# Optimization experiments

Hardware: AMD Instinct MI355X
Metric: run time of the kernel (lower is better)

Reference implementation:

```python
import jax, jax.numpy as jnp
import numpy as np

D_MODEL = 1024
N_HEADS = 16
D_K = D_MODEL // N_HEADS


def setup_inputs() -> dict:
    key = jax.random.key(0)
    ks = jax.random.split(key, 9)
    B, S = 2, 2048
    scale = 1.0 / np.sqrt(D_MODEL)
    inp = {
        "X": jax.random.normal(ks[0], (B, S, D_MODEL), dtype=jnp.float32),
        "Wq": jax.random.normal(ks[1], (D_MODEL, D_MODEL), dtype=jnp.float32) * scale,
        "bq": jnp.zeros((D_MODEL,), dtype=jnp.float32),
        "Wk": jax.random.normal(ks[2], (D_MODEL, D_MODEL), dtype=jnp.float32) * scale,
        "bk": jnp.zeros((D_MODEL,), dtype=jnp.float32),
        "Wv": jax.random.normal(ks[3], (D_MODEL, D_MODEL), dtype=jnp.float32) * scale,
        "bv": jnp.zeros((D_MODEL,), dtype=jnp.float32),
        "Wo": jax.random.normal(ks[4], (D_MODEL, D_MODEL), dtype=jnp.float32) * scale,
        "bo": jnp.zeros((D_MODEL,), dtype=jnp.float32),
    }
    return inp


def reference(X, Wq, bq, Wk, bk, Wv, bv, Wo, bo):
    B, S, _ = X.shape
    # QKV projections (torch Linear: x @ W.T + b; here W stored as [in, out])
    Q = X @ Wq + bq
    K = X @ Wk + bk
    V = X @ Wv + bv
    # [B, S, H, Dk] -> [B, H, S, Dk]
    def split_heads(t):
        return t.reshape(B, S, N_HEADS, D_K).transpose(0, 2, 1, 3)
    Q, K, V = split_heads(Q), split_heads(K), split_heads(V)
    scores = jnp.einsum('bhqd,bhkd->bhqk', Q, K) / jnp.sqrt(jnp.float32(D_K))
    attn = jax.nn.softmax(scores, axis=-1)
    out = jnp.einsum('bhqk,bhkd->bhqd', attn, V)  # [B, H, S, Dk]
    out = out.transpose(0, 2, 1, 3).reshape(B, S, D_MODEL)
    return out @ Wo + bo
```

## Files before the change

### kernel.cpp

```cpp
#include <hip/hip_runtime.h>
#include <hip/hip_bf16.h>


typedef __attribute__((ext_vector_type(8))) short short8;
typedef __attribute__((ext_vector_type(4))) float f32x4;
typedef unsigned short u16;
typedef unsigned int u32;

static __device__ __forceinline__ u16 f2bf(float f) {
    union { float f; u32 u; } c; c.f = f;
    u32 u = c.u;
    u32 r = u + 0x7fffu + ((u >> 16) & 1u);
    return (u16)(r >> 16);
}
static __device__ __forceinline__ float bf2f(u16 x) {
    union { u32 u; float f; } c; c.u = ((u32)x) << 16;
    return c.f;
}

#define GL1(p) ((const __attribute__((address_space(1))) void*)(p))
#define LD3(p) ((__attribute__((address_space(3))) void*)(p))
static __device__ __forceinline__ void gld16(const void* g, void* l) {
    __builtin_amdgcn_global_load_lds(GL1(g), LD3(l), 16, 0, 0);
}

#define Q_PRESCALE 0.18033688011112042f

__global__ __launch_bounds__(256) void prep(
    const float* __restrict__ X, u16* __restrict__ Xb,
    const float* __restrict__ W0, const float* __restrict__ W1,
    const float* __restrict__ W2, const float* __restrict__ W3,
    u16* __restrict__ T0, u16* __restrict__ T1,
    u16* __restrict__ T2, u16* __restrict__ T3)
{
    int id = blockIdx.x;
    int t = threadIdx.x;
    if (id >= 1024) {
        int i = (id - 1024) * 1024 + t * 4;
        float4 v = *reinterpret_cast<const float4*>(X + i);
        ushort4 o;
        o.x = f2bf(v.x); o.y = f2bf(v.y); o.z = f2bf(v.z); o.w = f2bf(v.w);
        *reinterpret_cast<ushort4*>(Xb + i) = o;
        return;
    }
    const float* W; u16* T;
    switch (id >> 8) {
        case 0: W = W0; T = T0; break;
        case 1: W = W1; T = T1; break;
        case 2: W = W2; T = T2; break;
        default: W = W3; T = T3; break;
    }
    int rem = id & 255;
    int n0 = (rem & 15) * 64, k0 = (rem >> 4) * 64;
    __shared__ float tile[64][65];
    int r = t / 16, c4 = (t % 16) * 4;
    #pragma unroll
    for (int p = 0; p < 4; p++) {
        int row = p * 16 + r;
        float4 v = *reinterpret_cast<const float4*>(W + (k0 + row) * 1024 + n0 + c4);
        tile[row][c4 + 0] = v.x; tile[row][c4 + 1] = v.y;
        tile[row][c4 + 2] = v.z; tile[row][c4 + 3] = v.w;
    }
    __syncthreads();
    #pragma unroll
    for (int p = 0; p < 4; p++) {
        int nrow = p * 16 + r;
        ushort4 o;
        o.x = f2bf(tile[c4 + 0][nrow]); o.y = f2bf(tile[c4 + 1][nrow]);
        o.z = f2bf(tile[c4 + 2][nrow]); o.w = f2bf(tile[c4 + 3][nrow]);
        *reinterpret_cast<ushort4*>(T + (n0 + nrow) * 1024 + k0 + c4) = o;
    }
}

__global__ __launch_bounds__(256) void gemm_qkv(
    const u16* __restrict__ Xb,
    const u16* __restrict__ Wtq, const u16* __restrict__ Wtk, const u16* __restrict__ Wtv,
    const float* __restrict__ bq, const float* __restrict__ bk, const float* __restrict__ bv,
    u16* __restrict__ Qn, u16* __restrict__ Kn, u16* __restrict__ Vtg)
{
    const u16* Wt; const float* bias;
    if (blockIdx.z == 0)      { Wt = Wtq; bias = bq; }
    else if (blockIdx.z == 1) { Wt = Wtk; bias = bk; }
    else                      { Wt = Wtv; bias = bv; }

    __shared__ __align__(16) u16 As[128 * 32];
    __shared__ __align__(16) u16 Bs[128 * 32];
    int t = threadIdx.x;
    int w = t >> 6, lane = t & 63, l15 = lane & 15, quad = lane >> 4;
    int wm = (w >> 1) * 64, wn = (w & 1) * 64;
    int row0 = blockIdx.y * 128, col0 = blockIdx.x * 128;

    int drow = lane >> 2;
    int gc8 = ((lane & 3) ^ (drow & 3) ^ ((drow >> 2) & 3)) * 8;
    int asw = ((quad ^ (l15 & 3) ^ ((l15 >> 2) & 3)) & 3) * 8;

    f32x4 acc[4][4];
    #pragma unroll
    for (int i = 0; i < 4; i++)
        #pragma unroll
        for (int j = 0; j < 4; j++)
            acc[i][j] = (f32x4){0.f, 0.f, 0.f, 0.f};

    for (int k0 = 0; k0 < 1024; k0 += 32) {
        __syncthreads();
        #pragma unroll
        for (int q = 0; q < 2; q++) {
            int rr = w * 32 + q * 16;
            gld16(&Xb[(row0 + rr + drow) * 1024 + k0 + gc8], &As[rr * 32]);
            gld16(&Wt[(col0 + rr + drow) * 1024 + k0 + gc8], &Bs[rr * 32]);
        }
        __syncthreads();
        short8 a[4], b[4];
        #pragma unroll
        for (int i = 0; i < 4; i++)
            a[i] = *reinterpret_cast<const short8*>(&As[(wm + i * 16 + l15) * 32 + asw]);
        #pragma unroll
        for (int j = 0; j < 4; j++)
            b[j] = *reinterpret_cast<const short8*>(&Bs[(wn + j * 16 + l15) * 32 + asw]);
        #pragma unroll
        for (int i = 0; i < 4; i++)
            #pragma unroll
            for (int j = 0; j < 4; j++)
                acc[i][j] = __builtin_amdgcn_mfma_f32_16x16x32_bf16(a[i], b[j], acc[i][j], 0, 0, 0);
    }

    if (blockIdx.z == 2) {
        #pragma unroll
        for (int i = 0; i < 4; i++) {
            int gr = row0 + wm + i * 16 + quad * 4;
            int b_ = gr >> 11, s = gr & 2047;
            #pragma unroll
            for (int j = 0; j < 4; j++) {
                int col = col0 + wn + j * 16 + l15;
                int h = col >> 6, d = col & 63;
                float bb = bias[col];
                ushort4 pk;
                pk.x = f2bf(acc[i][j][0] + bb);
                pk.y = f2bf(acc[i][j][1] + bb);
                pk.z = f2bf(acc[i][j][2] + bb);
                pk.w = f2bf(acc[i][j][3] + bb);
                *reinterpret_cast<ushort4*>(&Vtg[((b_ * 16 + h) * 64 + d) * 2048 + s]) = pk;
            }
        }
    } else {
        u16* dst = (blockIdx.z == 0) ? Qn : Kn;
        float osc = (blockIdx.z == 0) ? Q_PRESCALE : 1.0f;
        #pragma unroll
        for (int i = 0; i < 4; i++) {
            int rowb = row0 + wm + i * 16 + quad * 4;
            #pragma unroll
            for (int j = 0; j < 4; j++) {
                int col = col0 + wn + j * 16 + l15;
                float bb = bias[col];
                #pragma unroll
                for (int r = 0; r < 4; r++)
                    dst[(rowb + r) * 1024 + col] = f2bf((acc[i][j][r] + bb) * osc);
            }
        }
    }
}

__global__ __launch_bounds__(256) void attn(
    const u16* __restrict__ Qn, const u16* __restrict__ Kn,
    const u16* __restrict__ Vtg, u16* __restrict__ Opart, float* __restrict__ Lsum)
{
    int qt = blockIdx.x, bh = blockIdx.y, sp = blockIdx.z;
    int b_ = bh >> 4, h = bh & 15;
    const u16* Vp = Vtg + bh * (64 * 2048);
    u16* Op = Opart + sp * (4096 * 1024);
    float* Lp = Lsum + sp * (32 * 2048) + bh * 2048;

    __shared__ __align__(16) u16 Ks[64 * 64];
    __shared__ __align__(16) u16 Vt[64 * 64];
    __shared__ __align__(16) u16 Ps[128 * 64];

    int t = threadIdx.x, w = t >> 6, lane = t & 63, l15 = lane & 15, quad = lane >> 4;

    short8 qf[2][2];
    #pragma unroll
    for (int f = 0; f < 2; f++)
        #pragma unroll
        for (int ds = 0; ds < 2; ds++)
            qf[f][ds] = *reinterpret_cast<const short8*>(
                &Qn[(b_ * 2048 + qt * 128 + w * 32 + f * 16 + l15) * 1024 +
                    h * 64 + ds * 32 + quad * 8]);

    int di = lane >> 3;
    int dc8 = ((lane & 7) ^ di) * 8;

    int rl = l15 & 7, rh = l15 >> 3;
    int koff[4][2];
    #pragma unroll
    for (int j = 0; j < 4; j++)
        #pragma unroll
        for (int ds = 0; ds < 2; ds++)
            koff[j][ds] = (j * 2 + rh) * 512 + rl * 64 + (((ds * 4 + quad) ^ rl) & 7) * 8;

    int pwt[2][4];
    #pragma unroll
    for (int f = 0; f < 2; f++)
        #pragma unroll
        for (int j = 0; j < 4; j++)
            pwt[f][j] = (w * 32 + f * 16 + l15) * 64 +
                        (((2 * j + (quad >> 1)) ^ rl) * 8) + (quad & 1) * 4;
    int prt[2][2];
    #pragma unroll
    for (int f = 0; f < 2; f++)
        #pragma unroll
        for (int ks = 0; ks < 2; ks++)
            prt[f][ks] = (w * 32 + f * 16 + l15) * 64 + (((4 * ks + quad) ^ rl) * 8);

    f32x4 acc[2][4];
    float lsum[2] = {0.f, 0.f};
    #pragma unroll
    for (int f = 0; f < 2; f++)
        #pragma unroll
        for (int j = 0; j < 4; j++) acc[f][j] = (f32x4){0.f, 0.f, 0.f, 0.f};

    for (int kt = 0; kt < 16; kt++) {
        int kbase = sp * 1024 + kt * 64;
        __syncthreads();
        #pragma unroll
        for (int sg = 0; sg < 2; sg++) {
            int seg = w * 2 + sg;
            gld16(&Kn[(b_ * 2048 + kbase + seg * 8 + di) * 1024 + h * 64 + dc8],
                  &Ks[seg * 512]);
            gld16(&Vp[(seg * 8 + di) * 2048 + kbase + dc8], &Vt[seg * 512]);
        }
        __syncthreads();

        f32x4 sc[2][4];
        #pragma unroll
        for (int j = 0; j < 4; j++) {
            f32x4 s0 = (f32x4){0.f, 0.f, 0.f, 0.f};
            f32x4 s1 = (f32x4){0.f, 0.f, 0.f, 0.f};
            #pragma unroll
            for (int ds = 0; ds < 2; ds++) {
                short8 kf = *reinterpret_cast<const short8*>(&Ks[koff[j][ds]]);
                s0 = __builtin_amdgcn_mfma_f32_16x16x32_bf16(kf, qf[0][ds], s0, 0, 0, 0);
                s1 = __builtin_amdgcn_mfma_f32_16x16x32_bf16(kf, qf[1][ds], s1, 0, 0, 0);
            }
            sc[0][j] = s0; sc[1][j] = s1;
        }

        #pragma unroll
        for (int f = 0; f < 2; f++)
            #pragma unroll
            for (int j = 0; j < 4; j++) {
                float p0 = __builtin_amdgcn_exp2f(sc[f][j][0]);
                float p1 = __builtin_amdgcn_exp2f(sc[f][j][1]);
                float p2 = __builtin_amdgcn_exp2f(sc[f][j][2]);
                float p3 = __builtin_amdgcn_exp2f(sc[f][j][3]);
                lsum[f] += (p0 + p1) + (p2 + p3);
                union { float fv; u32 uv; } c0, c1, c2, c3;
                c0.fv = p0; c1.fv = p1; c2.fv = p2; c3.fv = p3;
                uint2 pk;
                pk.x = (c0.uv >> 16) | (c1.uv & 0xffff0000u);
                pk.y = (c2.uv >> 16) | (c3.uv & 0xffff0000u);
                *reinterpret_cast<uint2*>(&Ps[pwt[f][j]]) = pk;
            }

        #pragma unroll
        for (int ks = 0; ks < 2; ks++) {
            short8 pf0 = *reinterpret_cast<const short8*>(&Ps[prt[0][ks]]);
            short8 pf1 = *reinterpret_cast<const short8*>(&Ps[prt[1][ks]]);
            #pragma unroll
            for (int j = 0; j < 4; j++) {
                short8 vf = *reinterpret_cast<const short8*>(&Vt[koff[j][ks]]);
                acc[0][j] = __builtin_amdgcn_mfma_f32_16x16x32_bf16(pf0, vf, acc[0][j], 0, 0, 0);
                acc[1][j] = __builtin_amdgcn_mfma_f32_16x16x32_bf16(pf1, vf, acc[1][j], 0, 0, 0);
            }
        }
    }

    #pragma unroll
    for (int f = 0; f < 2; f++) {
        float s = lsum[f];
        s += __shfl_xor(s, 16);
        s += __shfl_xor(s, 32);
        lsum[f] = s;
    }
    if (quad == 0) {
        #pragma unroll
        for (int f = 0; f < 2; f++)
            Lp[qt * 128 + w * 32 + f * 16 + l15] = lsum[f];
    }

    #pragma unroll
    for (int f = 0; f < 2; f++)
        #pragma unroll
        for (int j = 0; j < 4; j++)
            #pragma unroll
            for (int r = 0; r < 4; r++) {
                int srow = qt * 128 + w * 32 + f * 16 + quad * 4 + r;
                Op[(b_ * 2048 + srow) * 1024 + h * 64 + j * 16 + l15] = f2bf(acc[f][j][r]);
            }
}

__global__ __launch_bounds__(256) void combine(
    const u16* __restrict__ O0, const u16* __restrict__ O1,
    const float* __restrict__ L0, const float* __restrict__ L1,
    u16* __restrict__ Ob)
{
    int idx8 = (blockIdx.x * 256 + threadIdx.x) * 8;
    int row = idx8 >> 10, col = idx8 & 1023;
    int b_ = row >> 11, s = row & 2047, h = col >> 6;
    int li = (b_ * 16 + h) * 2048 + s;
    float inv = 1.0f / (L0[li] + L1[li]);
    union { uint4 v; u16 s[8]; } ua, ub, uo;
    ua.v = *reinterpret_cast<const uint4*>(&O0[idx8]);
    ub.v = *reinterpret_cast<const uint4*>(&O1[idx8]);
    #pragma unroll
    for (int i = 0; i < 8; i++)
        uo.s[i] = f2bf((bf2f(ua.s[i]) + bf2f(ub.s[i])) * inv);
    *reinterpret_cast<uint4*>(&Ob[idx8]) = uo.v;
}

__global__ __launch_bounds__(256) void gemm_out(
    const u16* __restrict__ Ob, const u16* __restrict__ Wto,
    const float* __restrict__ bo, float* __restrict__ out)
{
    __shared__ __align__(16) u16 As[128 * 32];
    __shared__ __align__(16) u16 Bs[128 * 32];
    int t = threadIdx.x;
    int w = t >> 6, lane = t & 63, l15 = lane & 15, quad = lane >> 4;
    int wm = (w >> 1) * 64, wn = (w & 1) * 64;
    int row0 = blockIdx.y * 128, col0 = blockIdx.x * 128;

    int drow = lane >> 2;
    int gc8 = ((lane & 3) ^ (drow & 3) ^ ((drow >> 2) & 3)) * 8;
    int asw = ((quad ^ (l15 & 3) ^ ((l15 >> 2) & 3)) & 3) * 8;

    f32x4 acc[4][4];
    #pragma unroll
    for (int i = 0; i < 4; i++)
        #pragma unroll
        for (int j = 0; j < 4; j++)
            acc[i][j] = (f32x4){0.f, 0.f, 0.f, 0.f};

    for (int k0 = 0; k0 < 1024; k0 += 32) {
        __syncthreads();
        #pragma unroll
        for (int q = 0; q < 2; q++) {
            int rr = w * 32 + q * 16;
            gld16(&Ob[(row0 + rr + drow) * 1024 + k0 + gc8], &As[rr * 32]);
            gld16(&Wto[(col0 + rr + drow) * 1024 + k0 + gc8], &Bs[rr * 32]);
        }
        __syncthreads();
        short8 a[4], b[4];
        #pragma unroll
        for (int i = 0; i < 4; i++)
            a[i] = *reinterpret_cast<const short8*>(&As[(wm + i * 16 + l15) * 32 + asw]);
        #pragma unroll
        for (int j = 0; j < 4; j++)
            b[j] = *reinterpret_cast<const short8*>(&Bs[(wn + j * 16 + l15) * 32 + asw]);
        #pragma unroll
        for (int i = 0; i < 4; i++)
            #pragma unroll
            for (int j = 0; j < 4; j++)
                acc[i][j] = __builtin_amdgcn_mfma_f32_16x16x32_bf16(a[i], b[j], acc[i][j], 0, 0, 0);
    }
    #pragma unroll
    for (int i = 0; i < 4; i++) {
        int rowb = row0 + wm + i * 16 + quad * 4;
        #pragma unroll
        for (int j = 0; j < 4; j++) {
            int col = col0 + wn + j * 16 + l15;
            float bb = bo[col];
            #pragma unroll
            for (int r = 0; r < 4; r++)
                out[(rowb + r) * 1024 + col] = acc[i][j][r] + bb;
        }
    }
}

extern "C" void kernel_launch(void* const* d_in, const int* in_sizes, int n_in,
                              void* d_out, int out_size, void* d_ws, size_t ws_size,
                              hipStream_t stream) {
    const float* X  = (const float*)d_in[0];
    const float* Wq = (const float*)d_in[1];
    const float* bq = (const float*)d_in[2];
    const float* Wk = (const float*)d_in[3];
    const float* bk = (const float*)d_in[4];
    const float* Wv = (const float*)d_in[5];
    const float* bv = (const float*)d_in[6];
    const float* Wo = (const float*)d_in[7];
    const float* bo = (const float*)d_in[8];
    float* out = (float*)d_out;

    char* ws = (char*)d_ws;
    u16* Xb   = (u16*)(ws);
    u16* Wtq  = (u16*)(ws + (8u  << 20));
    u16* Wtk  = (u16*)(ws + (10u << 20));
    u16* Wtv  = (u16*)(ws + (12u << 20));
    u16* Wto  = (u16*)(ws + (14u << 20));
    u16* Qn   = (u16*)(ws + (16u << 20));
    u16* Kn   = (u16*)(ws + (24u << 20));
    u16* Vtg  = (u16*)(ws + (32u << 20));
    u16* Op   = (u16*)(ws + (40u << 20));
    float* Ls = (float*)(ws + (56u << 20));
    u16* Ob   = (u16*)(ws + (57u << 20));

    prep     <<<5120, 256, 0, stream>>>(X, Xb, Wq, Wk, Wv, Wo, Wtq, Wtk, Wtv, Wto);
    gemm_qkv <<<dim3(8, 32, 3), 256, 0, stream>>>(Xb, Wtq, Wtk, Wtv, bq, bk, bv, Qn, Kn, Vtg);
    attn     <<<dim3(16, 32, 2), 256, 0, stream>>>(Qn, Kn, Vtg, Op, Ls);
    combine  <<<2048, 256, 0, stream>>>(Op, Op + (4096 * 1024), Ls, Ls + (32 * 2048), Ob);
    gemm_out <<<dim3(8, 32), 256, 0, stream>>>(Ob, Wto, bo, out);
}
```

Measured before the change: 234.2 us.

## Double-buffer LDS tiles, fuse QKV GEMM, and store Q/K head-major

Converts the QKV GEMM, output GEMM and attention K/V loops to a double-buffered LDS scheme with one barrier per iteration, prefetching the next tile while computing the current one. Concatenates Wq/Wk/Wv into one transposed matrix with the Q scale folded into weights and bias, launching a flat 1D grid. Q and K are written in [B,H,S,Dk] layout so attention loads contiguous per-head rows. Uses more LDS per block and relies on the barrier's implicit wait for async global-to-LDS loads.

Result: faster. 212.1 us (-9.4%).

```diff
diff --git a/kernel.cpp b/kernel.cpp
--- a/kernel.cpp
+++ b/kernel.cpp
@@ -28,13 +28,22 @@
 
 __global__ __launch_bounds__(256) void prep(
     const float* __restrict__ X, u16* __restrict__ Xb,
-    const float* __restrict__ W0, const float* __restrict__ W1,
-    const float* __restrict__ W2, const float* __restrict__ W3,
-    u16* __restrict__ T0, u16* __restrict__ T1,
-    u16* __restrict__ T2, u16* __restrict__ T3)
+    const float* __restrict__ Wq, const float* __restrict__ Wk,
+    const float* __restrict__ Wv, const float* __restrict__ Wo,
+    const float* __restrict__ bq, const float* __restrict__ bk,
+    const float* __restrict__ bv,
+    u16* __restrict__ Wqkv, u16* __restrict__ Wto, float* __restrict__ Bp)
 {
     int id = blockIdx.x;
     int t = threadIdx.x;
+    if (id == 5120) {
+        for (int i = t; i < 3072; i += 256) {
+            int wsel = i >> 10, c = i & 1023;
+            float v = (wsel == 0) ? bq[c] * Q_PRESCALE : (wsel == 1 ? bk[c] : bv[c]);
+            Bp[i] = v;
+        }
+        return;
+    }
     if (id >= 1024) {
         int i = (id - 1024) * 1024 + t * 4;
         float4 v = *reinterpret_cast<const float4*>(X + i);
@@ -43,12 +52,13 @@
         *reinterpret_cast<ushort4*>(Xb + i) = o;
         return;
     }
-    const float* W; u16* T;
-    switch (id >> 8) {
-        case 0: W = W0; T = T0; break;
-        case 1: W = W1; T = T1; break;
-        case 2: W = W2; T = T2; break;
-        default: W = W3; T = T3; break;
+    int which = id >> 8;
+    const float* W; u16* T; float sc;
+    switch (which) {
+        case 0: W = Wq; T = Wqkv;                sc = Q_PRESCALE; break;
+        case 1: W = Wk; T = Wqkv + 1024 * 1024;  sc = 1.0f; break;
+        case 2: W = Wv; T = Wqkv + 2048 * 1024;  sc = 1.0f; break;
+        default: W = Wo; T = Wto;                sc = 1.0f; break;
     }
     int rem = id & 255;
     int n0 = (rem & 15) * 64, k0 = (rem >> 4) * 64;
@@ -58,8 +68,8 @@
     for (int p = 0; p < 4; p++) {
         int row = p * 16 + r;
         float4 v = *reinterpret_cast<const float4*>(W + (k0 + row) * 1024 + n0 + c4);
-        tile[row][c4 + 0] = v.x; tile[row][c4 + 1] = v.y;
-        tile[row][c4 + 2] = v.z; tile[row][c4 + 3] = v.w;
+        tile[row][c4 + 0] = v.x * sc; tile[row][c4 + 1] = v.y * sc;
+        tile[row][c4 + 2] = v.z * sc; tile[row][c4 + 3] = v.w * sc;
     }
     __syncthreads();
     #pragma unroll
@@ -72,28 +82,26 @@
     }
 }
 
-__global__ __launch_bounds__(256) void gemm_qkv(
-    const u16* __restrict__ Xb,
-    const u16* __restrict__ Wtq, const u16* __restrict__ Wtk, const u16* __restrict__ Wtv,
-    const float* __restrict__ bq, const float* __restrict__ bk, const float* __restrict__ bv,
-    u16* __restrict__ Qn, u16* __restrict__ Kn, u16* __restrict__ Vtg)
+__global__ __launch_bounds__(256, 3) void gemm_qkv(
+    const u16* __restrict__ Xb, const u16* __restrict__ Wqkv,
+    const float* __restrict__ Bp,
+    u16* __restrict__ Qb, u16* __restrict__ Kb, u16* __restrict__ Vtg)
 {
-    const u16* Wt; const float* bias;
-    if (blockIdx.z == 0)      { Wt = Wtq; bias = bq; }
-    else if (blockIdx.z == 1) { Wt = Wtk; bias = bk; }
-    else                      { Wt = Wtv; bias = bv; }
-
-    __shared__ __align__(16) u16 As[128 * 32];
-    __shared__ __align__(16) u16 Bs[128 * 32];
+    __shared__ __align__(16) u16 As[2][128 * 32];
+    __shared__ __align__(16) u16 Bs[2][128 * 32];
     int t = threadIdx.x;
     int w = t >> 6, lane = t & 63, l15 = lane & 15, quad = lane >> 4;
     int wm = (w >> 1) * 64, wn = (w & 1) * 64;
-    int row0 = blockIdx.y * 128, col0 = blockIdx.x * 128;
+    int bid = blockIdx.x;
+    int row0 = (bid / 24) * 128, col0 = (bid % 24) * 128;
 
     int drow = lane >> 2;
     int gc8 = ((lane & 3) ^ (drow & 3) ^ ((drow >> 2) & 3)) * 8;
     int asw = ((quad ^ (l15 & 3) ^ ((l15 >> 2) & 3)) & 3) * 8;
 
+    const u16* Ag = Xb + (row0 + drow) * 1024 + gc8;
+    const u16* Bg = Wqkv + (col0 + drow) * 1024 + gc8;
+
     f32x4 acc[4][4];
     #pragma unroll
     for (int i = 0; i < 4; i++)
@@ -101,22 +109,31 @@
         for (int j = 0; j < 4; j++)
             acc[i][j] = (f32x4){0.f, 0.f, 0.f, 0.f};
 
-    for (int k0 = 0; k0 < 1024; k0 += 32) {
+    #pragma unroll
+    for (int q = 0; q < 2; q++) {
+        int rr = w * 32 + q * 16;
+        gld16(Ag + rr * 1024, &As[0][rr * 32]);
+        gld16(Bg + rr * 1024, &Bs[0][rr * 32]);
+    }
+    for (int kt = 0; kt < 32; kt++) {
         __syncthreads();
-        #pragma unroll
-        for (int q = 0; q < 2; q++) {
-            int rr = w * 32 + q * 16;
-            gld16(&Xb[(row0 + rr + drow) * 1024 + k0 + gc8], &As[rr * 32]);
-            gld16(&Wt[(col0 + rr + drow) * 1024 + k0 + gc8], &Bs[rr * 32]);
-        }
-        __syncthreads();
+        int cur = kt & 1;
+        if (kt < 31) {
+            int k0 = (kt + 1) * 32;
+            #pragma unroll
+            for (int q = 0; q < 2; q++) {
+                int rr = w * 32 + q * 16;
+                gld16(Ag + rr * 1024 + k0, &As[cur ^ 1][rr * 32]);
+                gld16(Bg + rr * 1024 + k0, &Bs[cur ^ 1][rr * 32]);
+            }
+        }
         short8 a[4], b[4];
         #pragma unroll
         for (int i = 0; i < 4; i++)
-            a[i] = *reinterpret_cast<const short8*>(&As[(wm + i * 16 + l15) * 32 + asw]);
-        #pragma unroll
-        for (int j = 0; j < 4; j++)
-            b[j] = *reinterpret_cast<const short8*>(&Bs[(wn + j * 16 + l15) * 32 + asw]);
+            a[i] = *reinterpret_cast<const short8*>(&As[cur][(wm + i * 16 + l15) * 32 + asw]);
+        #pragma unroll
+        for (int j = 0; j < 4; j++)
+            b[j] = *reinterpret_cast<const short8*>(&Bs[cur][(wn + j * 16 + l15) * 32 + asw]);
         #pragma unroll
         for (int i = 0; i < 4; i++)
             #pragma unroll
@@ -124,7 +141,8 @@
                 acc[i][j] = __builtin_amdgcn_mfma_f32_16x16x32_bf16(a[i], b[j], acc[i][j], 0, 0, 0);
     }
 
-    if (blockIdx.z == 2) {
+    int osel = col0 >> 10;
+    if (osel == 2) {
         #pragma unroll
         for (int i = 0; i < 4; i++) {
             int gr = row0 + wm + i * 16 + quad * 4;
@@ -132,8 +150,8 @@
             #pragma unroll
             for (int j = 0; j < 4; j++) {
                 int col = col0 + wn + j * 16 + l15;
-                int h = col >> 6, d = col & 63;
-                float bb = bias[col];
+                int c = col & 1023, h = c >> 6, d = c & 63;
+                float bb = Bp[col];
                 ushort4 pk;
                 pk.x = f2bf(acc[i][j][0] + bb);
                 pk.y = f2bf(acc[i][j][1] + bb);
@@ -143,35 +161,40 @@
             }
         }
     } else {
-        u16* dst = (blockIdx.z == 0) ? Qn : Kn;
-        float osc = (blockIdx.z == 0) ? Q_PRESCALE : 1.0f;
+        u16* dst = osel ? Kb : Qb;
         #pragma unroll
         for (int i = 0; i < 4; i++) {
             int rowb = row0 + wm + i * 16 + quad * 4;
             #pragma unroll
             for (int j = 0; j < 4; j++) {
                 int col = col0 + wn + j * 16 + l15;
-                float bb = bias[col];
+                int c = col & 1023, h = c >> 6, d = c & 63;
+                float bb = Bp[col];
                 #pragma unroll
-                for (int r = 0; r < 4; r++)
-                    dst[(rowb + r) * 1024 + col] = f2bf((acc[i][j][r] + bb) * osc);
+                for (int r = 0; r < 4; r++) {
+                    int gr = rowb + r;
+                    int b_ = gr >> 11, s = gr & 2047;
+                    dst[(((b_ << 4) + h) * 2048 + s) * 64 + d] = f2bf(acc[i][j][r] + bb);
+                }
             }
         }
     }
 }
 
 __global__ __launch_bounds__(256) void attn(
-    const u16* __restrict__ Qn, const u16* __restrict__ Kn,
+    const u16* __restrict__ Qb, const u16* __restrict__ Kb,
     const u16* __restrict__ Vtg, u16* __restrict__ Opart, float* __restrict__ Lsum)
 {
     int qt = blockIdx.x, bh = blockIdx.y, sp = blockIdx.z;
     int b_ = bh >> 4, h = bh & 15;
+    const u16* Qp = Qb + bh * (2048 * 64);
+    const u16* Kp = Kb + bh * (2048 * 64);
     const u16* Vp = Vtg + bh * (64 * 2048);
     u16* Op = Opart + sp * (4096 * 1024);
     float* Lp = Lsum + sp * (32 * 2048) + bh * 2048;
 
-    __shared__ __align__(16) u16 Ks[64 * 64];
-    __shared__ __align__(16) u16 Vt[64 * 64];
+    __shared__ __align__(16) u16 Ks[2][64 * 64];
+    __shared__ __align__(16) u16 Vt[2][64 * 64];
     __shared__ __align__(16) u16 Ps[128 * 64];
 
     int t = threadIdx.x, w = t >> 6, lane = t & 63, l15 = lane & 15, quad = lane >> 4;
@@ -182,8 +205,7 @@
         #pragma unroll
         for (int ds = 0; ds < 2; ds++)
             qf[f][ds] = *reinterpret_cast<const short8*>(
-                &Qn[(b_ * 2048 + qt * 128 + w * 32 + f * 16 + l15) * 1024 +
-                    h * 64 + ds * 32 + quad * 8]);
+                &Qp[(qt * 128 + w * 32 + f * 16 + l15) * 64 + ds * 32 + quad * 8]);
 
     int di = lane >> 3;
     int dc8 = ((lane & 7) ^ di) * 8;
@@ -217,17 +239,25 @@
         #pragma unroll
         for (int j = 0; j < 4; j++) acc[f][j] = (f32x4){0.f, 0.f, 0.f, 0.f};
 
+    int kb0 = sp * 1024;
+    #pragma unroll
+    for (int sg = 0; sg < 2; sg++) {
+        int seg = w * 2 + sg;
+        gld16(&Kp[(kb0 + seg * 8 + di) * 64 + dc8], &Ks[0][seg * 512]);
+        gld16(&Vp[(seg * 8 + di) * 2048 + kb0 + dc8], &Vt[0][seg * 512]);
+    }
     for (int kt = 0; kt < 16; kt++) {
-        int kbase = sp * 1024 + kt * 64;
         __syncthreads();
-        #pragma unroll
-        for (int sg = 0; sg < 2; sg++) {
-            int seg = w * 2 + sg;
-            gld16(&Kn[(b_ * 2048 + kbase + seg * 8 + di) * 1024 + h * 64 + dc8],
-                  &Ks[seg * 512]);
-            gld16(&Vp[(seg * 8 + di) * 2048 + kbase + dc8], &Vt[seg * 512]);
-        }
-        __syncthreads();
+        int cur = kt & 1;
+        if (kt < 15) {
+            int kbase = kb0 + (kt + 1) * 64;
+            #pragma unroll
+            for (int sg = 0; sg < 2; sg++) {
+                int seg = w * 2 + sg;
+                gld16(&Kp[(kbase + seg * 8 + di) * 64 + dc8], &Ks[cur ^ 1][seg * 512]);
+                gld16(&Vp[(seg * 8 + di) * 2048 + kbase + dc8], &Vt[cur ^ 1][seg * 512]);
+            }
+        }
 
         f32x4 sc[2][4];
         #pragma unroll
@@ -236,7 +266,7 @@
             f32x4 s1 = (f32x4){0.f, 0.f, 0.f, 0.f};
             #pragma unroll
             for (int ds = 0; ds < 2; ds++) {
-                short8 kf = *reinterpret_cast<const short8*>(&Ks[koff[j][ds]]);
+                short8 kf = *reinterpret_cast<const short8*>(&Ks[cur][koff[j][ds]]);
                 s0 = __builtin_amdgcn_mfma_f32_16x16x32_bf16(kf, qf[0][ds], s0, 0, 0, 0);
                 s1 = __builtin_amdgcn_mfma_f32_16x16x32_bf16(kf, qf[1][ds], s1, 0, 0, 0);
             }
@@ -266,7 +296,7 @@
             short8 pf1 = *reinterpret_cast<const short8*>(&Ps[prt[1][ks]]);
             #pragma unroll
             for (int j = 0; j < 4; j++) {
-                short8 vf = *reinterpret_cast<const short8*>(&Vt[koff[j][ks]]);
+                short8 vf = *reinterpret_cast<const short8*>(&Vt[cur][koff[j][ks]]);
                 acc[0][j] = __builtin_amdgcn_mfma_f32_16x16x32_bf16(pf0, vf, acc[0][j], 0, 0, 0);
                 acc[1][j] = __builtin_amdgcn_mfma_f32_16x16x32_bf16(pf1, vf, acc[1][j], 0, 0, 0);
             }
@@ -316,12 +346,12 @@
     *reinterpret_cast<uint4*>(&Ob[idx8]) = uo.v;
 }
 
-__global__ __launch_bounds__(256) void gemm_out(
+__global__ __launch_bounds__(256, 3) void gemm_out(
     const u16* __restrict__ Ob, const u16* __restrict__ Wto,
     const float* __restrict__ bo, float* __restrict__ out)
 {
-    __shared__ __align__(16) u16 As[128 * 32];
-    __shared__ __align__(16) u16 Bs[128 * 32];
+    __shared__ __align__(16) u16 As[2][128 * 32];
+    __shared__ __align__(16) u16 Bs[2][128 * 32];
     int t = threadIdx.x;
     int w = t >> 6, lane = t & 63, l15 = lane & 15, quad = lane >> 4;
     int wm = (w >> 1) * 64, wn = (w & 1) * 64;
@@ -331,6 +361,9 @@
     int gc8 = ((lane & 3) ^ (drow & 3) ^ ((drow >> 2) & 3)) * 8;
     int asw = ((quad ^ (l15 & 3) ^ ((l15 >> 2) & 3)) & 3) * 8;
 
+    const u16* Ag = Ob + (row0 + drow) * 1024 + gc8;
+    const u16* Bg = Wto + (col0 + drow) * 1024 + gc8;
+
     f32x4 acc[4][4];
     #pragma unroll
     for (int i = 0; i < 4; i++)
@@ -338,22 +371,31 @@
         for (int j = 0; j < 4; j++)
             acc[i][j] = (f32x4){0.f, 0.f, 0.f, 0.f};
 
-    for (int k0 = 0; k0 < 1024; k0 += 32) {
+    #pragma unroll
+    for (int q = 0; q < 2; q++) {
+        int rr = w * 32 + q * 16;
+        gld16(Ag + rr * 1024, &As[0][rr * 32]);
+        gld16(Bg + rr * 1024, &Bs[0][rr * 32]);
+    }
+    for (int kt = 0; kt < 32; kt++) {
         __syncthreads();
-        #pragma unroll
-        for (int q = 0; q < 2; q++) {
-            int rr = w * 32 + q * 16;
-            gld16(&Ob[(row0 + rr + drow) * 1024 + k0 + gc8], &As[rr * 32]);
-            gld16(&Wto[(col0 + rr + drow) * 1024 + k0 + gc8], &Bs[rr * 32]);
-        }
-        __syncthreads();
+        int cur = kt & 1;
+        if (kt < 31) {
+            int k0 = (kt + 1) * 32;
+            #pragma unroll
+            for (int q = 0; q < 2; q++) {
+                int rr = w * 32 + q * 16;
+                gld16(Ag + rr * 1024 + k0, &As[cur ^ 1][rr * 32]);
+                gld16(Bg + rr * 1024 + k0, &Bs[cur ^ 1][rr * 32]);
+            }
+        }
         short8 a[4], b[4];
         #pragma unroll
         for (int i = 0; i < 4; i++)
-            a[i] = *reinterpret_cast<const short8*>(&As[(wm + i * 16 + l15) * 32 + asw]);
-        #pragma unroll
-        for (int j = 0; j < 4; j++)
-            b[j] = *reinterpret_cast<const short8*>(&Bs[(wn + j * 16 + l15) * 32 + asw]);
+            a[i] = *reinterpret_cast<const short8*>(&As[cur][(wm + i * 16 + l15) * 32 + asw]);
+        #pragma unroll
+        for (int j = 0; j < 4; j++)
+            b[j] = *reinterpret_cast<const short8*>(&Bs[cur][(wn + j * 16 + l15) * 32 + asw]);
         #pragma unroll
         for (int i = 0; i < 4; i++)
             #pragma unroll
@@ -389,21 +431,20 @@
     float* out = (float*)d_out;
 
     char* ws = (char*)d_ws;
-    u16* Xb   = (u16*)(ws);
-    u16* Wtq  = (u16*)(ws + (8u  << 20));
-    u16* Wtk  = (u16*)(ws + (10u << 20));
-    u16* Wtv  = (u16*)(ws + (12u << 20));
-    u16* Wto  = (u16*)(ws + (14u << 20));
-    u16* Qn   = (u16*)(ws + (16u << 20));
-    u16* Kn   = (u16*)(ws + (24u << 20));
-    u16* Vtg  = (u16*)(ws + (32u << 20));
-    u16* Op   = (u16*)(ws + (40u << 20));
-    float* Ls = (float*)(ws + (56u << 20));
-    u16* Ob   = (u16*)(ws + (57u << 20));
-
-    prep     <<<5120, 256, 0, stream>>>(X, Xb, Wq, Wk, Wv, Wo, Wtq, Wtk, Wtv, Wto);
-    gemm_qkv <<<dim3(8, 32, 3), 256, 0, stream>>>(Xb, Wtq, Wtk, Wtv, bq, bk, bv, Qn, Kn, Vtg);
-    attn     <<<dim3(16, 32, 2), 256, 0, stream>>>(Qn, Kn, Vtg, Op, Ls);
+    u16* Xb    = (u16*)(ws);
+    u16* Ob    = (u16*)(ws);
+    u16* Wqkv  = (u16*)(ws + (8u  << 20));
+    u16* Wto   = (u16*)(ws + (14u << 20));
+    float* Bp  = (float*)(ws + (16u << 20));
+    u16* Qb    = (u16*)(ws + (17u << 20));
+    u16* Kb    = (u16*)(ws + (25u << 20));
+    u16* Vtg   = (u16*)(ws + (33u << 20));
+    u16* Op    = (u16*)(ws + (41u << 20));
+    float* Ls  = (float*)(ws + (57u << 20));
+
+    prep     <<<5121, 256, 0, stream>>>(X, Xb, Wq, Wk, Wv, Wo, bq, bk, bv, Wqkv, Wto, Bp);
+    gemm_qkv <<<768, 256, 0, stream>>>(Xb, Wqkv, Bp, Qb, Kb, Vtg);
+    attn     <<<dim3(16, 32, 2), 256, 0, stream>>>(Qb, Kb, Vtg, Op, Ls);
     combine  <<<2048, 256, 0, stream>>>(Op, Op + (4096 * 1024), Ls, Ls + (32 * 2048), Ob);
     gemm_out <<<dim3(8, 32), 256, 0, stream>>>(Ob, Wto, bo, out);
 }
```
